# Kernel optimization log

Measured on AMD Instinct MI355X. Metric: run time of the kernel, lower is better.

## Reference

```python
import jax, jax.numpy as jnp
import numpy as np

EMB = 2048
HEADS = 16
HEAD = EMB // HEADS


def setup_inputs() -> dict:
    key = jax.random.key(0)
    ks = jax.random.split(key, 10)
    B, S = 4, 2048
    x = jax.random.normal(ks[0], (B, S, EMB), dtype=jnp.float32)
    # additive causal mask: 0 on/below diagonal, -inf above
    neg_inf = jnp.finfo(jnp.float32).min
    attn_mask = jnp.where(jnp.tril(jnp.ones((S, S), dtype=bool)), 0.0, neg_inf).astype(jnp.float32)
    scale = 1.0 / np.sqrt(EMB)  # xavier-ish init scale
    Wq = jax.random.normal(ks[1], (EMB, EMB), dtype=jnp.float32) * scale
    Wk = jax.random.normal(ks[2], (EMB, EMB), dtype=jnp.float32) * scale
    Wv = jax.random.normal(ks[3], (EMB, EMB), dtype=jnp.float32) * scale
    Wo = jax.random.normal(ks[4], (EMB, EMB), dtype=jnp.float32) * scale
    bq = jnp.zeros((EMB,), dtype=jnp.float32)
    bk = jnp.zeros((EMB,), dtype=jnp.float32)
    bv = jnp.zeros((EMB,), dtype=jnp.float32)
    bo = jnp.zeros((EMB,), dtype=jnp.float32)
    return {"x": x, "attn_mask": attn_mask, "Wq": Wq, "bq": bq, "Wk": Wk, "bk": bk,
            "Wv": Wv, "bv": bv, "Wo": Wo, "bo": bo}


def reference(x, attn_mask, Wq, bq, Wk, bk, Wv, bv, Wo, bo):
    B, S, E = x.shape
    # torch Linear: y = x @ W.T + b
    def proj(W, b):
        y = jnp.einsum('bse,fe->bsf', x, W) + b
        return y.reshape(B, S, HEADS, HEAD).transpose(0, 2, 1, 3)  # [B,H,S,D]
    q = proj(Wq, bq)
    k = proj(Wk, bk)
    v = proj(Wv, bv)
    scores = jnp.einsum('bhqd,bhkd->bhqk', q, k) / np.sqrt(HEAD)
    scores = scores + attn_mask  # broadcast [S,S] over [B,H,S,S]
    attn = jax.nn.softmax(scores, axis=-1)  # dropout p=0.0 -> identity
    ctx = jnp.einsum('bhqk,bhkd->bhqd', attn, v)
    ctx = ctx.transpose(0, 2, 1, 3).reshape(B, S, E)
    out = jnp.einsum('bse,fe->bsf', ctx, Wo) + bo
    return out
```

## Files before the change

### kernel.cpp

```cpp
#include <hip/hip_runtime.h>

#define BATCH 4
#define SEQ   2048
#define EMBD  2048
#define NHEAD 16
#define HEADD 128

#define GM (BATCH*SEQ)
#define GN EMBD
#define GK EMBD

typedef __attribute__((ext_vector_type(8))) short short8;
typedef __attribute__((ext_vector_type(4))) short s16x4;
typedef __attribute__((ext_vector_type(4))) float f32x4;

static __device__ __forceinline__ short f2bf(float f) {
  unsigned u = __builtin_bit_cast(unsigned, f);
  unsigned r = (u + 0x7fffu + ((u >> 16) & 1u)) >> 16;
  return (short)r;
}

static __device__ __forceinline__ void glds16(const short* g, short* l) {
  __builtin_amdgcn_global_load_lds(
      (const __attribute__((address_space(1))) unsigned int*)g,
      (__attribute__((address_space(3))) unsigned int*)l, 16, 0, 0);
}

__global__ __launch_bounds__(256) void cvt_f32_bf16(
    const float* __restrict__ in, short* __restrict__ out, int n)
{
  int i = (blockIdx.x * 256 + threadIdx.x) * 8;
  if (i + 7 < n) {
    float4 a = *(const float4*)&in[i];
    float4 b = *(const float4*)&in[i + 4];
    short8 o;
    o[0] = f2bf(a.x); o[1] = f2bf(a.y); o[2] = f2bf(a.z); o[3] = f2bf(a.w);
    o[4] = f2bf(b.x); o[5] = f2bf(b.y); o[6] = f2bf(b.z); o[7] = f2bf(b.w);
    *(short8*)&out[i] = o;
  }
}

__global__ __launch_bounds__(256) void cvt_w4(
    const float* __restrict__ w0, const float* __restrict__ w1,
    const float* __restrict__ w2, const float* __restrict__ w3,
    short* __restrict__ o0, short* __restrict__ o1,
    short* __restrict__ o2, short* __restrict__ o3)
{
  const float* src = blockIdx.y == 0 ? w0 : blockIdx.y == 1 ? w1 : blockIdx.y == 2 ? w2 : w3;
  short*       dst = blockIdx.y == 0 ? o0 : blockIdx.y == 1 ? o1 : blockIdx.y == 2 ? o2 : o3;
  int i = (blockIdx.x * 256 + threadIdx.x) * 8;
  float4 a = *(const float4*)&src[i];
  float4 b = *(const float4*)&src[i + 4];
  short8 o;
  o[0] = f2bf(a.x); o[1] = f2bf(a.y); o[2] = f2bf(a.z); o[3] = f2bf(a.w);
  o[4] = f2bf(b.x); o[5] = f2bf(b.y); o[6] = f2bf(b.z); o[7] = f2bf(b.w);
  *(short8*)&dst[i] = o;
}

template<bool F32OUT>
__global__ __launch_bounds__(256) void gemm_bias_kernel(
    const short* __restrict__ A, const short* __restrict__ W,
    const float* __restrict__ bias, void* __restrict__ Cout)
{
  __shared__ short As[128 * 64];
  __shared__ short Bs[128 * 64];
  const int tid  = threadIdx.x;
  const int lane = tid & 63;
  const int wv   = tid >> 6;
  const int quad = lane >> 4;
  const int l15  = lane & 15;
  const int m0 = blockIdx.y * 128;
  const int n0 = blockIdx.x * 128;
  const int wm = (wv >> 1) * 64;
  const int wn = (wv & 1) * 64;

  const f32x4 zerov = {0.f, 0.f, 0.f, 0.f};
  f32x4 acc[4][4];
#pragma unroll
  for (int mi = 0; mi < 4; ++mi)
#pragma unroll
    for (int ni = 0; ni < 4; ++ni) acc[mi][ni] = zerov;

  for (int k0 = 0; k0 < GK; k0 += 64) {
#pragma unroll
    for (int rr = 0; rr < 4; ++rr) {
      int c   = rr * 4 + wv;
      int g   = c * 64 + lane;
      int row = g >> 3;
      int col8 = (g & 7) ^ (row & 7);
      glds16(&A[(size_t)(m0 + row) * GK + k0 + col8 * 8], &As[c * 512]);
      glds16(&W[(size_t)(n0 + row) * GK + k0 + col8 * 8], &Bs[c * 512]);
    }
    __syncthreads();
#pragma unroll
    for (int ks = 0; ks < 2; ++ks) {
      short8 af[4], bfr[4];
#pragma unroll
      for (int mi = 0; mi < 4; ++mi) {
        int row = wm + mi * 16 + l15;
        af[mi] = *(const short8*)&As[(row * 8 + ((ks * 4 + quad) ^ (row & 7))) * 8];
      }
#pragma unroll
      for (int ni = 0; ni < 4; ++ni) {
        int row = wn + ni * 16 + l15;
        bfr[ni] = *(const short8*)&Bs[(row * 8 + ((ks * 4 + quad) ^ (row & 7))) * 8];
      }
#pragma unroll
      for (int mi = 0; mi < 4; ++mi)
#pragma unroll
        for (int ni = 0; ni < 4; ++ni)
          acc[mi][ni] = __builtin_amdgcn_mfma_f32_16x16x32_bf16(af[mi], bfr[ni], acc[mi][ni], 0, 0, 0);
    }
    __syncthreads();
  }

#pragma unroll
  for (int mi = 0; mi < 4; ++mi) {
    int mg = m0 + wm + mi * 16 + quad * 4;
#pragma unroll
    for (int ni = 0; ni < 4; ++ni) {
      int ng = n0 + wn + ni * 16 + l15;
      float bv = bias[ng];
#pragma unroll
      for (int r = 0; r < 4; ++r) {
        float val = acc[mi][ni][r] + bv;
        if (F32OUT)
          ((float*)Cout)[(size_t)(mg + r) * GN + ng] = val;
        else
          ((short*)Cout)[(size_t)(mg + r) * GN + ng] = f2bf(val);
      }
    }
  }
}

__global__ __launch_bounds__(256) void transpose_v(
    const short* __restrict__ V, short* __restrict__ Vt)
{
  __shared__ short T[64][72];
  const int b  = blockIdx.z;
  const int n0 = blockIdx.x * 64;
  const int s0 = blockIdx.y * 64;
#pragma unroll
  for (int rr = 0; rr < 2; ++rr) {
    int c = rr * 256 + threadIdx.x;
    int srow = c >> 3;
    int ncol = (c & 7) << 3;
    *(short8*)&T[srow][ncol] = *(const short8*)&V[((size_t)b * SEQ + s0 + srow) * EMBD + n0 + ncol];
  }
  __syncthreads();
#pragma unroll
  for (int rr = 0; rr < 2; ++rr) {
    int c = rr * 256 + threadIdx.x;
    int nrow = c >> 3;
    int scol = (c & 7) << 3;
    short8 o;
#pragma unroll
    for (int j = 0; j < 8; ++j) o[j] = T[scol + j][nrow];
    *(short8*)&Vt[((size_t)b * EMBD + n0 + nrow) * SEQ + s0 + scol] = o;
  }
}

__global__ __launch_bounds__(256) void flash_attn(
    const short* __restrict__ Q, const short* __restrict__ K,
    const short* __restrict__ Vt, short* __restrict__ Ctx)
{
  __shared__ short Ksf[2][64 * 128];
  __shared__ short Vsf[2][128 * 64];
  __shared__ short Ps[4][16][72];

  const int bid  = blockIdx.x;
  const int slot = bid >> 3;
  const int grp  = ((bid & 7) << 3) | (slot >> 4);
  const int xq   = slot & 15;
  const int h = grp & 15, b = grp >> 4;

  const int tid = threadIdx.x, lane = tid & 63, wv = tid >> 6;
  const int quad = lane >> 4, l15 = lane & 15;

  const size_t bhq    = (size_t)b * SEQ * EMBD + (size_t)h * HEADD;
  const size_t vtbase = ((size_t)b * EMBD + (size_t)h * HEADD) * SEQ;
  const float SL2E = 0.08838834764831845f * 1.4426950408889634f;
  const int NQT = SEQ / 64;

  int kco[4], koff[4], voff[4];
#pragma unroll
  for (int rr = 0; rr < 4; ++rr) {
    int c = rr * 4 + wv;
    int g = c * 64 + lane;
    kco[rr] = c * 512;
    { int row = g >> 4, col16 = (g & 15) ^ (row & 15);
      koff[rr] = row * EMBD + col16 * 8; }
    { int row = g >> 3, col8 = (g & 7) ^ (row & 7);
      voff[rr] = row * SEQ + col8 * 8; }
  }

#define STAGE(buf, kt_) do {                                                 \
    const short* kb_ = &K[bhq + (size_t)((kt_) * 64) * EMBD];                \
    const short* vb_ = &Vt[vtbase + (size_t)((kt_) * 64)];                   \
    _Pragma("unroll")                                                        \
    for (int rr = 0; rr < 4; ++rr) {                                         \
      glds16(&kb_[koff[rr]], &Ksf[buf][kco[rr]]);                            \
      glds16(&vb_[voff[rr]], &Vsf[buf][kco[rr]]);                            \
    }                                                                        \
  } while (0)

  const f32x4 zerov = {0.f, 0.f, 0.f, 0.f};

  for (int pass = 0; pass < 2; ++pass) {
    const int qt = pass ? (NQT - 1 - xq) : xq;
    const int qg    = qt * 64 + wv * 16 + l15;
    const int rowg0 = qt * 64 + wv * 16 + quad * 4;

    short8 qf[4];
#pragma unroll
    for (int ks = 0; ks < 4; ++ks)
      qf[ks] = *(const short8*)&Q[bhq + (size_t)qg * EMBD + ks * 32 + quad * 8];

    f32x4 oacc[8];
#pragma unroll
    for (int ni = 0; ni < 8; ++ni) oacc[ni] = zerov;
    float m_s = -INFINITY;
    float l_s = 0.f;

    __syncthreads();
    STAGE(0, 0);

    for (int kt = 0; kt <= qt; ++kt) {
      const int cur = kt & 1;
      __syncthreads();
      if (kt < qt) STAGE(cur ^ 1, kt + 1);

      f32x4 sA[4];
#pragma unroll
      for (int ni = 0; ni < 4; ++ni) sA[ni] = zerov;
#pragma unroll
      for (int ks = 0; ks < 4; ++ks)
#pragma unroll
        for (int ni = 0; ni < 4; ++ni) {
          int row = ni * 16 + l15;
          short8 kf = *(const short8*)&Ksf[cur][(row * 16 + ((ks * 4 + quad) ^ (row & 15))) * 8];
          sA[ni] = __builtin_amdgcn_mfma_f32_16x16x32_bf16(kf, qf[ks], sA[ni], 0, 0, 0);
        }

      if (kt == qt) {
        const int key00 = kt * 64;
#pragma unroll
        for (int ni = 0; ni < 4; ++ni)
#pragma unroll
          for (int r = 0; r < 4; ++r) {
            int keyg = key00 + ni * 16 + quad * 4 + r;
            if (keyg > qg) sA[ni][r] = -INFINITY;
          }
      }

      float mv = sA[0][0];
#pragma unroll
      for (int ni = 0; ni < 4; ++ni)
#pragma unroll
        for (int r = 0; r < 4; ++r)
          if (ni | r) mv = fmaxf(mv, sA[ni][r]);
      mv = fmaxf(mv, __shfl_xor(mv, 16, 64));
      mv = fmaxf(mv, __shfl_xor(mv, 32, 64));
      float mn = fmaxf(m_s, mv);
      float alpha = exp2f((m_s - mn) * SL2E);
      m_s = mn;
      float msl = mn * SL2E;
      float sum = 0.f;
#pragma unroll
      for (int ni = 0; ni < 4; ++ni)
#pragma unroll
        for (int r = 0; r < 4; ++r) {
          float p = exp2f(sA[ni][r] * SL2E - msl);
          sA[ni][r] = p;
          sum += p;
        }
      sum += __shfl_xor(sum, 16, 64);
      sum += __shfl_xor(sum, 32, 64);
      l_s = l_s * alpha + sum;

      float al[4];
#pragma unroll
      for (int r = 0; r < 4; ++r) al[r] = __shfl(alpha, quad * 4 + r, 16);
#pragma unroll
      for (int ni = 0; ni < 8; ++ni)
#pragma unroll
        for (int r = 0; r < 4; ++r) oacc[ni][r] *= al[r];

#pragma unroll
      for (int ni = 0; ni < 4; ++ni) {
        s16x4 pk;
#pragma unroll
        for (int r = 0; r < 4; ++r) pk[r] = f2bf(sA[ni][r]);
        *(s16x4*)&Ps[wv][l15][ni * 16 + quad * 4] = pk;
      }

      short8 pf[2];
#pragma unroll
      for (int ks = 0; ks < 2; ++ks)
        pf[ks] = *(const short8*)&Ps[wv][l15][ks * 32 + quad * 8];
#pragma unroll
      for (int ni = 0; ni < 8; ++ni)
#pragma unroll
        for (int ks = 0; ks < 2; ++ks) {
          int row = ni * 16 + l15;
          short8 vf = *(const short8*)&Vsf[cur][(row * 8 + ((ks * 4 + quad) ^ (row & 7))) * 8];
          oacc[ni] = __builtin_amdgcn_mfma_f32_16x16x32_bf16(pf[ks], vf, oacc[ni], 0, 0, 0);
        }
    }

    float linv = 1.0f / l_s;
    float iv[4];
#pragma unroll
    for (int r = 0; r < 4; ++r) iv[r] = __shfl(linv, quad * 4 + r, 16);
#pragma unroll
    for (int r = 0; r < 4; ++r)
#pragma unroll
      for (int ni = 0; ni < 8; ++ni)
        Ctx[bhq + (size_t)(rowg0 + r) * EMBD + ni * 16 + l15] = f2bf(oacc[ni][r] * iv[r]);
  }
#undef STAGE
}

extern "C" void kernel_launch(void* const* d_in, const int* in_sizes, int n_in,
                              void* d_out, int out_size, void* d_ws, size_t ws_size,
                              hipStream_t stream)
{
  const float* x  = (const float*)d_in[0];
  const float* Wq = (const float*)d_in[2];
  const float* bq = (const float*)d_in[3];
  const float* Wk = (const float*)d_in[4];
  const float* bk = (const float*)d_in[5];
  const float* Wv = (const float*)d_in[6];
  const float* bv = (const float*)d_in[7];
  const float* Wo = (const float*)d_in[8];
  const float* bo = (const float*)d_in[9];
  float* out = (float*)d_out;

  const size_t NE = (size_t)BATCH * SEQ * EMBD;
  const size_t NW = (size_t)EMBD * EMBD;
  short* xb  = (short*)d_ws;
  short* wqb = xb  + NE;
  short* wkb = wqb + NW;
  short* wvb = wkb + NW;
  short* wob = wvb + NW;
  short* q   = wob + NW;
  short* k   = q   + NE;
  short* v   = k   + NE;
  short* vt  = v   + NE;
  short* ctx = v;

  cvt_f32_bf16<<<NE / (256 * 8), 256, 0, stream>>>(x, xb, (int)NE);
  cvt_w4<<<dim3(NW / (256 * 8), 4), 256, 0, stream>>>(Wq, Wk, Wv, Wo, wqb, wkb, wvb, wob);

  dim3 gg(GN / 128, GM / 128);
  gemm_bias_kernel<false><<<gg, 256, 0, stream>>>(xb, wqb, bq, q);
  gemm_bias_kernel<false><<<gg, 256, 0, stream>>>(xb, wkb, bk, k);
  gemm_bias_kernel<false><<<gg, 256, 0, stream>>>(xb, wvb, bv, v);
  transpose_v<<<dim3(EMBD / 64, SEQ / 64, BATCH), 256, 0, stream>>>(v, vt);
  flash_attn<<<dim3((SEQ / 128) * NHEAD * BATCH), 256, 0, stream>>>(q, k, vt, ctx);
  gemm_bias_kernel<true><<<gg, 256, 0, stream>>>(ctx, wob, bo, out);
}
```

Baseline: 669.1 us.

## Retile GEMMs to 256x256 with 4-stage async pipeline; lazy softmax rescale in attention

```diff
diff --git a/kernel.cpp b/kernel.cpp
--- a/kernel.cpp
+++ b/kernel.cpp
@@ -18,6 +18,12 @@
   unsigned u = __builtin_bit_cast(unsigned, f);
   unsigned r = (u + 0x7fffu + ((u >> 16) & 1u)) >> 16;
   return (short)r;
+}
+
+static __device__ __forceinline__ unsigned cvt_pk_bf16(float lo, float hi) {
+  unsigned r;
+  asm("v_cvt_pk_bf16_f32 %0, %1, %2" : "=v"(r) : "v"(lo), "v"(hi));
+  return r;
 }
 
 static __device__ __forceinline__ void glds16(const short* g, short* l) {
@@ -57,69 +63,100 @@
   *(short8*)&dst[i] = o;
 }
 
+#define BKT 32
+#define NTILES (GK / BKT)
+
 template<bool F32OUT>
-__global__ __launch_bounds__(256) void gemm_bias_kernel(
+__global__ __launch_bounds__(512, 2) void gemm_bias_kernel(
     const short* __restrict__ A, const short* __restrict__ W,
     const float* __restrict__ bias, void* __restrict__ Cout)
 {
-  __shared__ short As[128 * 64];
-  __shared__ short Bs[128 * 64];
+  __shared__ short As[4][256 * 32];
+  __shared__ short Bs[4][256 * 32];
+
   const int tid  = threadIdx.x;
   const int lane = tid & 63;
   const int wv   = tid >> 6;
   const int quad = lane >> 4;
   const int l15  = lane & 15;
-  const int m0 = blockIdx.y * 128;
-  const int n0 = blockIdx.x * 128;
-  const int wm = (wv >> 1) * 64;
-  const int wn = (wv & 1) * 64;
-
+
+  const int bid = blockIdx.x;
+  const int swz = (bid & 7) * 32 + (bid >> 3);
+  const int n0 = (swz & 7) * 256;
+  const int m0 = (swz >> 3) * 256;
+
+  const int wm0 = (wv >> 2) * 128;
+  const int wn0 = (wv & 3) * 64;
+
+  size_t aoff[2], boff[2];
+#pragma unroll
+  for (int j = 0; j < 2; ++j) {
+    int g   = j * 512 + tid;
+    int row = g >> 2;
+    int cgl = (g & 3) ^ ((row & 3) ^ ((row >> 2) & 1));
+    aoff[j] = (size_t)(m0 + row) * GK + cgl * 8;
+    boff[j] = (size_t)(n0 + row) * GK + cgl * 8;
+  }
+
+#define GSTAGE(t_) do {                                                      \
+    int buf_ = (t_) & 3; int k0_ = (t_) * BKT;                               \
+    _Pragma("unroll")                                                        \
+    for (int j = 0; j < 2; ++j) {                                            \
+      glds16(&A[aoff[j] + k0_], &As[buf_][(j * 512 + wv * 64) * 8]);         \
+      glds16(&W[boff[j] + k0_], &Bs[buf_][(j * 512 + wv * 64) * 8]);         \
+    }                                                                        \
+  } while (0)
+
+  const int fsw = (l15 & 3) ^ ((l15 >> 2) & 1);
   const f32x4 zerov = {0.f, 0.f, 0.f, 0.f};
-  f32x4 acc[4][4];
-#pragma unroll
-  for (int mi = 0; mi < 4; ++mi)
+  f32x4 acc[8][4];
+#pragma unroll
+  for (int mi = 0; mi < 8; ++mi)
 #pragma unroll
     for (int ni = 0; ni < 4; ++ni) acc[mi][ni] = zerov;
 
-  for (int k0 = 0; k0 < GK; k0 += 64) {
-#pragma unroll
-    for (int rr = 0; rr < 4; ++rr) {
-      int c   = rr * 4 + wv;
-      int g   = c * 64 + lane;
-      int row = g >> 3;
-      int col8 = (g & 7) ^ (row & 7);
-      glds16(&A[(size_t)(m0 + row) * GK + k0 + col8 * 8], &As[c * 512]);
-      glds16(&W[(size_t)(n0 + row) * GK + k0 + col8 * 8], &Bs[c * 512]);
+  GSTAGE(0); GSTAGE(1); GSTAGE(2);
+
+  for (int t = 0; t < NTILES; ++t) {
+    if (t + 2 < NTILES)      asm volatile("s_waitcnt vmcnt(8)" ::: "memory");
+    else if (t + 1 < NTILES) asm volatile("s_waitcnt vmcnt(4)" ::: "memory");
+    else                     asm volatile("s_waitcnt vmcnt(0)" ::: "memory");
+    __builtin_amdgcn_sched_barrier(0);
+    __builtin_amdgcn_s_barrier();
+    __builtin_amdgcn_sched_barrier(0);
+    if (t + 3 < NTILES) GSTAGE(t + 3);
+    __builtin_amdgcn_sched_barrier(0);
+
+    const short* ap = &As[t & 3][0];
+    const short* bp = &Bs[t & 3][0];
+    short8 af[8], bfr[4];
+#pragma unroll
+    for (int mi = 0; mi < 8; ++mi) {
+      int row = wm0 + mi * 16 + l15;
+      af[mi] = *(const short8*)&ap[(row * 4 + (quad ^ fsw)) * 8];
     }
-    __syncthreads();
-#pragma unroll
-    for (int ks = 0; ks < 2; ++ks) {
-      short8 af[4], bfr[4];
-#pragma unroll
-      for (int mi = 0; mi < 4; ++mi) {
-        int row = wm + mi * 16 + l15;
-        af[mi] = *(const short8*)&As[(row * 8 + ((ks * 4 + quad) ^ (row & 7))) * 8];
-      }
-#pragma unroll
-      for (int ni = 0; ni < 4; ++ni) {
-        int row = wn + ni * 16 + l15;
-        bfr[ni] = *(const short8*)&Bs[(row * 8 + ((ks * 4 + quad) ^ (row & 7))) * 8];
-      }
-#pragma unroll
-      for (int mi = 0; mi < 4; ++mi)
-#pragma unroll
-        for (int ni = 0; ni < 4; ++ni)
-          acc[mi][ni] = __builtin_amdgcn_mfma_f32_16x16x32_bf16(af[mi], bfr[ni], acc[mi][ni], 0, 0, 0);
+#pragma unroll
+    for (int ni = 0; ni < 4; ++ni) {
+      int row = wn0 + ni * 16 + l15;
+      bfr[ni] = *(const short8*)&bp[(row * 4 + (quad ^ fsw)) * 8];
     }
-    __syncthreads();
-  }
-
-#pragma unroll
-  for (int mi = 0; mi < 4; ++mi) {
-    int mg = m0 + wm + mi * 16 + quad * 4;
+    __builtin_amdgcn_s_setprio(1);
+#pragma unroll
+    for (int mi = 0; mi < 8; ++mi)
+#pragma unroll
+      for (int ni = 0; ni < 4; ++ni)
+        acc[mi][ni] = __builtin_amdgcn_mfma_f32_16x16x32_bf16(af[mi], bfr[ni], acc[mi][ni], 0, 0, 0);
+    __builtin_amdgcn_s_setprio(0);
+    __builtin_amdgcn_sched_barrier(0);
+  }
+#undef GSTAGE
+
+#pragma unroll
+  for (int mi = 0; mi < 8; ++mi) {
+    int mg = m0 + wm0 + mi * 16 + quad * 4;
 #pragma unroll
     for (int ni = 0; ni < 4; ++ni) {
-      int ng = n0 + wn + ni * 16 + l15;
+      int ng = n0 + wn0 + ni * 16 + l15;
       float bv = bias[ng];
 #pragma unroll
       for (int r = 0; r < 4; ++r) {
@@ -180,6 +217,7 @@
   const size_t bhq    = (size_t)b * SEQ * EMBD + (size_t)h * HEADD;
   const size_t vtbase = ((size_t)b * EMBD + (size_t)h * HEADD) * SEQ;
   const float SL2E = 0.08838834764831845f * 1.4426950408889634f;
+  const float THRS = 8.0f / SL2E;
   const int NQT = SEQ / 64;
 
   int kco[4], koff[4], voff[4];
@@ -261,10 +299,22 @@
           if (ni | r) mv = fmaxf(mv, sA[ni][r]);
       mv = fmaxf(mv, __shfl_xor(mv, 16, 64));
       mv = fmaxf(mv, __shfl_xor(mv, 32, 64));
-      float mn = fmaxf(m_s, mv);
-      float alpha = exp2f((m_s - mn) * SL2E);
-      m_s = mn;
-      float msl = mn * SL2E;
+
+      if (!__all(mv <= m_s + THRS)) {
+        float mn = fmaxf(m_s, mv);
+        float alpha = exp2f((m_s - mn) * SL2E);
+        m_s = mn;
+        l_s *= alpha;
+        float al[4];
+#pragma unroll
+        for (int r = 0; r < 4; ++r) al[r] = __shfl(alpha, quad * 4 + r, 16);
+#pragma unroll
+        for (int ni = 0; ni < 8; ++ni)
+#pragma unroll
+          for (int r = 0; r < 4; ++r) oacc[ni][r] *= al[r];
+      }
+
+      float msl = m_s * SL2E;
       float sum = 0.f;
 #pragma unroll
       for (int ni = 0; ni < 4; ++ni)
@@ -276,22 +326,14 @@
         }
       sum += __shfl_xor(sum, 16, 64);
       sum += __shfl_xor(sum, 32, 64);
-      l_s = l_s * alpha + sum;
-
-      float al[4];
-#pragma unroll
-      for (int r = 0; r < 4; ++r) al[r] = __shfl(alpha, quad * 4 + r, 16);
-#pragma unroll
-      for (int ni = 0; ni < 8; ++ni)
-#pragma unroll
-        for (int r = 0; r < 4; ++r) oacc[ni][r] *= al[r];
+      l_s += sum;
 
 #pragma unroll
       for (int ni = 0; ni < 4; ++ni) {
-        s16x4 pk;
-#pragma unroll
-        for (int r = 0; r < 4; ++r) pk[r] = f2bf(sA[ni][r]);
-        *(s16x4*)&Ps[wv][l15][ni * 16 + quad * 4] = pk;
+        uint2 pk;
+        pk.x = cvt_pk_bf16(sA[ni][0], sA[ni][1]);
+        pk.y = cvt_pk_bf16(sA[ni][2], sA[ni][3]);
+        *(uint2*)&Ps[wv][l15][ni * 16 + quad * 4] = pk;
       }
 
       short8 pf[2];
@@ -352,11 +394,11 @@
   cvt_f32_bf16<<<NE / (256 * 8), 256, 0, stream>>>(x, xb, (int)NE);
   cvt_w4<<<dim3(NW / (256 * 8), 4), 256, 0, stream>>>(Wq, Wk, Wv, Wo, wqb, wkb, wvb, wob);
 
-  dim3 gg(GN / 128, GM / 128);
-  gemm_bias_kernel<false><<<gg, 256, 0, stream>>>(xb, wqb, bq, q);
-  gemm_bias_kernel<false><<<gg, 256, 0, stream>>>(xb, wkb, bk, k);
-  gemm_bias_kernel<false><<<gg, 256, 0, stream>>>(xb, wvb, bv, v);
+  dim3 gg((GM / 256) * (GN / 256));
+  gemm_bias_kernel<false><<<gg, 512, 0, stream>>>(xb, wqb, bq, q);
+  gemm_bias_kernel<false><<<gg, 512, 0, stream>>>(xb, wkb, bk, k);
+  gemm_bias_kernel<false><<<gg, 512, 0, stream>>>(xb, wvb, bv, v);
   transpose_v<<<dim3(EMBD / 64, SEQ / 64, BATCH), 256, 0, stream>>>(v, vt);
   flash_attn<<<dim3((SEQ / 128) * NHEAD * BATCH), 256, 0, stream>>>(q, k, vt, ctx);
-  gemm_bias_kernel<true><<<gg, 256, 0, stream>>>(ctx, wob, bo, out);
-}
+  gemm_bias_kernel<true><<<gg, 512, 0, stream>>>(ctx, wob, bo, out);
+}
```

After: 662.8 us. No clear change (-0.9%).
